# Optimization experiments

Measured on AMD Instinct MI355X. Metric: run time of the kernel, lower is better.

The kernel has to match this reference:

```python
import jax, jax.numpy as jnp
import numpy as np

D_MODEL = 1024
NUM_HEADS = 16
D_K = D_MODEL // NUM_HEADS


def setup_inputs() -> dict:
    key = jax.random.key(0)
    ks = jax.random.split(key, 6)
    B, S = 2, 2048
    scale = 1.0 / np.sqrt(D_MODEL)
    x = jax.random.normal(ks[0], (B, S, D_MODEL), dtype=jnp.float32)
    w_q = jax.random.normal(ks[1], (D_MODEL, D_MODEL), dtype=jnp.float32) * scale
    w_k = jax.random.normal(ks[2], (D_MODEL, D_MODEL), dtype=jnp.float32) * scale
    w_v = jax.random.normal(ks[3], (D_MODEL, D_MODEL), dtype=jnp.float32) * scale
    w_o = jax.random.normal(ks[4], (D_MODEL, D_MODEL), dtype=jnp.float32) * scale
    b_o = jax.random.normal(ks[5], (D_MODEL,), dtype=jnp.float32) * 0.01
    return {"x": x, "w_q": w_q, "w_k": w_k, "w_v": w_v, "w_o": w_o, "b_o": b_o}


def reference(x, w_q, w_k, w_v, w_o, b_o):
    B, S, _ = x.shape
    # Linear(d, d, bias=False): y = x @ W.T ; weights stored torch-style [out, in]
    def proj(w):
        y = jnp.einsum('bsd,ed->bse', x, w)
        return y.reshape(B, S, NUM_HEADS, D_K).transpose(0, 2, 1, 3)  # [B,H,S,Dk]
    Q, K, V = proj(w_q), proj(w_k), proj(w_v)
    scores = jnp.einsum('bhqd,bhkd->bhqk', Q, K) / np.sqrt(D_K)
    attn = jax.nn.softmax(scores, axis=-1)  # dropout p=0 (eval) -> identity
    out = jnp.einsum('bhqk,bhkd->bhqd', attn, V)
    out = out.transpose(0, 2, 1, 3).reshape(B, S, D_MODEL)
    return jnp.einsum('bsd,ed->bse', out, w_o) + b_o
```

## Files before the change

kernel.cpp:

```cpp
#include <hip/hip_runtime.h>
#include <hip/hip_bf16.h>


typedef __bf16 bf16x8 __attribute__((ext_vector_type(8)));
typedef float f32x4 __attribute__((ext_vector_type(4)));

__device__ __forceinline__ unsigned short f2bf(float f) {
  union { float f; unsigned int u; } c; c.f = f;
  unsigned int u = c.u;
  return (unsigned short)((u + 0x7FFFu + ((u >> 16) & 1u)) >> 16);
}

__device__ __forceinline__ unsigned int pk2bf(float a, float b) {
  union { float f; unsigned int u; } x, y;
  x.f = a; y.f = b;
  return __builtin_amdgcn_perm(y.u + 0x8000u, x.u + 0x8000u, 0x07060302u);
}

__device__ __forceinline__ bf16x8 ld_frag(const unsigned short* p) {
  union { uint4 u; bf16x8 b; } c;
  c.u = *(const uint4*)p;
  return c.b;
}

__device__ __forceinline__ uint4 cvt8(const float* __restrict__ p) {
  float4 a = *(const float4*)p;
  float4 b = *(const float4*)(p + 4);
  union { uint4 u; unsigned short s[8]; } r;
  r.s[0] = f2bf(a.x); r.s[1] = f2bf(a.y); r.s[2] = f2bf(a.z); r.s[3] = f2bf(a.w);
  r.s[4] = f2bf(b.x); r.s[5] = f2bf(b.y); r.s[6] = f2bf(b.z); r.s[7] = f2bf(b.w);
  return r.u;
}

typedef __attribute__((address_space(1))) const unsigned int as1_u32;
typedef __attribute__((address_space(3))) unsigned int as3_u32;
__device__ __forceinline__ void async16(const unsigned short* g,
                                        unsigned short* l) {
  __builtin_amdgcn_global_load_lds(
      (as1_u32*)(unsigned long long)g,
      (as3_u32*)(unsigned int)(unsigned long long)l, 16, 0, 0);
}

__global__ __launch_bounds__(256) void cvt_all(
    const float* __restrict__ s0, const float* __restrict__ s1,
    const float* __restrict__ s2, const float* __restrict__ s3,
    const float* __restrict__ s4,
    unsigned short* __restrict__ d0, unsigned short* __restrict__ d1,
    unsigned short* __restrict__ d2, unsigned short* __restrict__ d3,
    unsigned short* __restrict__ d4) {
  const float* srcs[5] = {s0, s1, s2, s3, s4};
  unsigned short* dsts[5] = {d0, d1, d2, d3, d4};
  const int ns[5] = {4194304, 1048576, 1048576, 1048576, 1048576};
  const int y = blockIdx.y;
  const int idx = (blockIdx.x * 256 + threadIdx.x) * 8;
  if (idx >= ns[y]) return;
  *(uint4*)(dsts[y] + idx) = cvt8(srcs[y] + idx);
}

template <int BM, bool OUT_F32>
__global__ __launch_bounds__(256) void gemm_bt(
    const unsigned short* __restrict__ A,
    const unsigned short* __restrict__ w0,
    const unsigned short* __restrict__ w1,
    const unsigned short* __restrict__ w2,
    const float* __restrict__ bias,
    void* __restrict__ outraw, float z0scale) {
  constexpr int NT = (BM == 128) ? 4 : 2;
  const int z = blockIdx.z;
  const unsigned short* W = (z == 0) ? w0 : ((z == 1) ? w1 : w2);
  const float scl = (z == 0) ? z0scale : 1.0f;

  __shared__ unsigned short a_lds[BM * 32];
  __shared__ unsigned short b_lds[128 * 32];

  const int tid = threadIdx.x;
  const int wave = tid >> 6, lane = tid & 63;
  const int quad = lane >> 4, l16 = lane & 15;
  const int wm = (BM == 128) ? (wave >> 1) * 64 : 0;
  const int wn = (BM == 128) ? (wave & 1) * 64 : wave * 32;
  const int bm = blockIdx.y * BM, bn = blockIdx.x * 128;

  const int rl = lane >> 2;
  const int kc = (lane & 3) ^ (rl & 3) ^ ((rl >> 2) & 3);
  const int arow = (BM == 128) ? (wave * 32 + rl) : (wave * 16 + rl);
  const unsigned short* ga = A + (size_t)(bm + arow) * 1024 + kc * 8;
  const unsigned short* gb = W + (size_t)(bn + wave * 32 + rl) * 1024 + kc * 8;
  unsigned short* la = &a_lds[arow - rl + 0] + 0;
  la = &a_lds[((BM == 128) ? wave * 32 : wave * 16) * 32];
  unsigned short* lb = &b_lds[wave * 32 * 32];

  const int rsw8 = ((l16 & 3) ^ ((l16 >> 2) & 3)) * 8;

  f32x4 acc[4][NT] = {};

  for (int k0 = 0; k0 < 1024; k0 += 32) {
    async16(ga, la);
    if (BM == 128) async16(ga + 16 * 1024, la + 16 * 32);
    async16(gb, lb);
    async16(gb + 16 * 1024, lb + 16 * 32);
    ga += 32; gb += 32;
    __syncthreads();

    bf16x8 af[4], bfr[NT];
#pragma unroll
    for (int t = 0; t < 4; ++t)
      af[t] = ld_frag(&a_lds[(wm + t * 16 + l16) * 32 + ((quad * 8) ^ rsw8)]);
#pragma unroll
    for (int t = 0; t < NT; ++t)
      bfr[t] = ld_frag(&b_lds[(wn + t * 16 + l16) * 32 + ((quad * 8) ^ rsw8)]);
#pragma unroll
    for (int mt = 0; mt < 4; ++mt)
#pragma unroll
      for (int nt = 0; nt < NT; ++nt)
        acc[mt][nt] = __builtin_amdgcn_mfma_f32_16x16x32_bf16(
            af[mt], bfr[nt], acc[mt][nt], 0, 0, 0);
    __syncthreads();
  }

#pragma unroll
  for (int nt = 0; nt < NT; ++nt) {
    const int n = bn + wn + nt * 16 + l16;
    const float bv = bias ? bias[n] : 0.0f;
#pragma unroll
    for (int mt = 0; mt < 4; ++mt)
#pragma unroll
      for (int r = 0; r < 4; ++r) {
        const int m = bm + wm + mt * 16 + quad * 4 + r;
        const float v = acc[mt][nt][r] * scl + bv;
        if (OUT_F32)
          ((float*)outraw)[(size_t)z * 4096 * 1024 + (size_t)m * 1024 + n] = v;
        else
          ((unsigned short*)outraw)[(size_t)z * 4096 * 1024 +
                                    (size_t)m * 1024 + n] = f2bf(v);
      }
  }
}

__global__ __launch_bounds__(256) void transpose_v(
    const unsigned short* __restrict__ v, unsigned short* __restrict__ vt) {
  const int st0 = blockIdx.x * 64;
  const int bh = blockIdx.y, b = bh >> 4, h = bh & 15;
  __shared__ unsigned short t[64 * 72];
  const int tid = threadIdx.x;
#pragma unroll
  for (int it = 0; it < 2; ++it) {
    const int c = it * 256 + tid;
    const int row = c >> 3, c8 = (c & 7) * 8;
    *(uint4*)&t[row * 72 + c8] =
        *(const uint4*)(v + (size_t)(b * 2048 + st0 + row) * 1024 + h * 64 + c8);
  }
  __syncthreads();
#pragma unroll
  for (int it = 0; it < 2; ++it) {
    const int c = it * 256 + tid;
    const int drow = c >> 3, s8 = (c & 7) * 8;
    union { uint4 u; unsigned short e[8]; } o;
#pragma unroll
    for (int j = 0; j < 8; ++j) o.e[j] = t[(s8 + j) * 72 + drow];
    *(uint4*)(vt + ((size_t)bh * 64 + drow) * 2048 + st0 + s8) = o.u;
  }
}

__global__ __launch_bounds__(256) void attn3(
    const unsigned short* __restrict__ qkv,
    const unsigned short* __restrict__ vt_g,
    unsigned short* __restrict__ ab) {
  constexpr size_t PL = (size_t)4096 * 1024;
  const int qt = blockIdx.x, bh = blockIdx.y;
  const int b = bh >> 4, h = bh & 15;

  __shared__ unsigned short kp[128 * 136];
  __shared__ unsigned short vtl[64 * 136];

  const int tid = threadIdx.x;
  const int wave = tid >> 6, lane = tid & 63;
  const int quad = lane >> 4, l16 = lane & 15;
  const int qb = quad * 20;

  const unsigned short* Kp = qkv + PL + ((size_t)b * 2048) * 1024 + h * 64;
  const unsigned short* Vt = vt_g + (size_t)bh * 64 * 2048;

  bf16x8 qf[2][2];
#pragma unroll
  for (int hf = 0; hf < 2; ++hf) {
    const unsigned short* qrow =
        qkv + (size_t)(b * 2048 + qt * 128 + wave * 32 + hf * 16 + l16) * 1024 +
        h * 64;
    union { uint4 u; bf16x8 bv; } c;
    c.u = *(const uint4*)(qrow + quad * 8);       qf[hf][0] = c.bv;
    c.u = *(const uint4*)(qrow + 32 + quad * 8);  qf[hf][1] = c.bv;
  }

  f32x4 o_acc[2][4] = {};
  float l_part[2] = {0.0f, 0.0f};

  for (int kv0 = 0; kv0 < 2048; kv0 += 128) {
    __syncthreads();
#pragma unroll
    for (int it = 0; it < 4; ++it) {
      const int c = it * 256 + tid;
      const int kr = c >> 3, kc = (c & 7) * 8;
      *(uint4*)&kp[kr * 72 + kc] =
          *(const uint4*)(Kp + (size_t)(kv0 + kr) * 1024 + kc);
      const int vr = c >> 4, vc = (c & 15) * 8;
      *(uint4*)&vtl[vr * 136 + vc] =
          *(const uint4*)(Vt + (size_t)vr * 2048 + kv0 + vc);
    }
    __syncthreads();

    f32x4 st[2][8] = {};
#pragma unroll
    for (int mb = 0; mb < 8; ++mb) {
      bf16x8 ak0 = ld_frag(&kp[(mb * 16 + l16) * 72 + quad * 8]);
      bf16x8 ak1 = ld_frag(&kp[(mb * 16 + l16) * 72 + 32 + quad * 8]);
#pragma unroll
      for (int hf = 0; hf < 2; ++hf) {
        st[hf][mb] = __builtin_amdgcn_mfma_f32_16x16x32_bf16(
            ak0, qf[hf][0], st[hf][mb], 0, 0, 0);
        st[hf][mb] = __builtin_amdgcn_mfma_f32_16x16x32_bf16(
            ak1, qf[hf][1], st[hf][mb], 0, 0, 0);
      }
    }

#pragma unroll
    for (int hf = 0; hf < 2; ++hf)
#pragma unroll
      for (int mb = 0; mb < 8; ++mb)
#pragma unroll
        for (int r = 0; r < 4; ++r) {
          const float p = __builtin_amdgcn_exp2f(st[hf][mb][r]);
          st[hf][mb][r] = p;
          l_part[hf] += p;
        }

    __syncthreads();
#pragma unroll
    for (int hf = 0; hf < 2; ++hf)
#pragma unroll
      for (int mb = 0; mb < 8; ++mb) {
        uint2 pk;
        pk.x = pk2bf(st[hf][mb][0], st[hf][mb][1]);
        pk.y = pk2bf(st[hf][mb][2], st[hf][mb][3]);
        *(uint2*)&kp[(wave * 32 + hf * 16 + l16) * 136 + mb * 16 + quad * 4] =
            pk;
      }

#pragma unroll
    for (int ks = 0; ks < 4; ++ks) {
      bf16x8 bvf[4];
#pragma unroll
      for (int nt = 0; nt < 4; ++nt)
        bvf[nt] = ld_frag(&vtl[(nt * 16 + l16) * 136 + ks * 32 + quad * 8]);
#pragma unroll
      for (int hf = 0; hf < 2; ++hf) {
        bf16x8 ap =
            ld_frag(&kp[(wave * 32 + hf * 16 + l16) * 136 + ks * 32 + quad * 8]);
#pragma unroll
        for (int nt = 0; nt < 4; ++nt)
          o_acc[hf][nt] = __builtin_amdgcn_mfma_f32_16x16x32_bf16(
              ap, bvf[nt], o_acc[hf][nt], 0, 0, 0);
      }
    }
  }

#pragma unroll
  for (int hf = 0; hf < 2; ++hf) {
    float lp = l_part[hf];
    lp += __shfl_xor(lp, 16);
    lp += __shfl_xor(lp, 32);
    float lr[4];
#pragma unroll
    for (int r = 0; r < 4; ++r) lr[r] = 1.0f / __shfl(lp, qb + r);
#pragma unroll
    for (int nt = 0; nt < 4; ++nt)
#pragma unroll
      for (int r = 0; r < 4; ++r) {
        const int row = qt * 128 + wave * 32 + hf * 16 + quad * 4 + r;
        ab[((size_t)b * 2048 + row) * 1024 + h * 64 + nt * 16 + l16] =
            f2bf(o_acc[hf][nt][r] * lr[r]);
      }
  }
}

extern "C" void kernel_launch(void* const* d_in, const int* in_sizes, int n_in,
                              void* d_out, int out_size, void* d_ws,
                              size_t ws_size, hipStream_t stream) {
  const float* x  = (const float*)d_in[0];
  const float* wq = (const float*)d_in[1];
  const float* wk = (const float*)d_in[2];
  const float* wv = (const float*)d_in[3];
  const float* wo = (const float*)d_in[4];
  const float* bo = (const float*)d_in[5];

  constexpr size_t PL = (size_t)4096 * 1024;
  unsigned short* qkv = (unsigned short*)d_ws;
  unsigned short* ab  = qkv + 2 * PL;
  unsigned short* xb  = qkv + 3 * PL;
  unsigned short* vt  = xb;
  unsigned short* wqb = qkv + 4 * PL;
  unsigned short* wkb = wqb + 1024 * 1024;
  unsigned short* wvb = wkb + 1024 * 1024;
  unsigned short* wob = wvb + 1024 * 1024;

  const float QSCALE = 0.18033688011112042f;

  cvt_all<<<dim3(2048, 5), 256, 0, stream>>>(x, wq, wk, wv, wo,
                                             xb, wqb, wkb, wvb, wob);
  gemm_bt<128, false><<<dim3(8, 32, 3), 256, 0, stream>>>(
      xb, wqb, wkb, wvb, nullptr, qkv, QSCALE);
  transpose_v<<<dim3(32, 32), 256, 0, stream>>>(qkv + 2 * PL, vt);
  attn3<<<dim3(16, 32), 256, 0, stream>>>(qkv, vt, ab);
  gemm_bt<64, true><<<dim3(8, 64, 1), 256, 0, stream>>>(
      ab, wob, wob, wob, bo, d_out, 1.0f);
}
```

Before: 222.4 us.

## Rewrite attention kernel with 32x32 MFMA, split-KV waves and register P

The attention kernel is restructured: each block now handles 64 queries, and its four waves split the KV sequence into two halves, combined at the end through shared memory. It uses 32x32x16 MFMAs, loads K/V tiles with async copies into XOR-swizzled LDS, and keeps the probabilities in registers using permlane32 swaps instead of writing them to LDS. The goal is to remove the P round-trip through LDS and the extra barriers, raise occupancy (launch bounds of 4, a smaller LDS footprint, twice as many blocks) and use wider MFMAs. The cost is a final cross-wave reduction step and more complex indexing.

```diff
diff --git a/kernel.cpp b/kernel.cpp
--- a/kernel.cpp
+++ b/kernel.cpp
@@ -4,6 +4,7 @@
 
 typedef __bf16 bf16x8 __attribute__((ext_vector_type(8)));
 typedef float f32x4 __attribute__((ext_vector_type(4)));
+typedef float f32x16 __attribute__((ext_vector_type(16)));
 
 __device__ __forceinline__ unsigned short f2bf(float f) {
   union { float f; unsigned int u; } c; c.f = f;
@@ -85,8 +86,7 @@
   const int arow = (BM == 128) ? (wave * 32 + rl) : (wave * 16 + rl);
   const unsigned short* ga = A + (size_t)(bm + arow) * 1024 + kc * 8;
   const unsigned short* gb = W + (size_t)(bn + wave * 32 + rl) * 1024 + kc * 8;
-  unsigned short* la = &a_lds[arow - rl + 0] + 0;
-  la = &a_lds[((BM == 128) ? wave * 32 : wave * 16) * 32];
+  unsigned short* la = &a_lds[((BM == 128) ? wave * 32 : wave * 16) * 32];
   unsigned short* lb = &b_lds[wave * 32 * 32];
 
   const int rsw8 = ((l16 & 3) ^ ((l16 >> 2) & 3)) * 8;
@@ -161,7 +161,7 @@
   }
 }
 
-__global__ __launch_bounds__(256) void attn3(
+__global__ __launch_bounds__(256, 4) void attn4(
     const unsigned short* __restrict__ qkv,
     const unsigned short* __restrict__ vt_g,
     unsigned short* __restrict__ ab) {
@@ -169,116 +169,121 @@
   const int qt = blockIdx.x, bh = blockIdx.y;
   const int b = bh >> 4, h = bh & 15;
 
-  __shared__ unsigned short kp[128 * 136];
-  __shared__ unsigned short vtl[64 * 136];
+  __shared__ __align__(16) unsigned short kvs[2][2][64 * 64];
+  __shared__ float sm_l[2][2][32];
 
   const int tid = threadIdx.x;
   const int wave = tid >> 6, lane = tid & 63;
-  const int quad = lane >> 4, l16 = lane & 15;
-  const int qb = quad * 20;
-
-  const unsigned short* Kp = qkv + PL + ((size_t)b * 2048) * 1024 + h * 64;
-  const unsigned short* Vt = vt_g + (size_t)bh * 64 * 2048;
-
-  bf16x8 qf[2][2];
-#pragma unroll
-  for (int hf = 0; hf < 2; ++hf) {
-    const unsigned short* qrow =
-        qkv + (size_t)(b * 2048 + qt * 128 + wave * 32 + hf * 16 + l16) * 1024 +
-        h * 64;
-    union { uint4 u; bf16x8 bv; } c;
-    c.u = *(const uint4*)(qrow + quad * 8);       qf[hf][0] = c.bv;
-    c.u = *(const uint4*)(qrow + 32 + quad * 8);  qf[hf][1] = c.bv;
-  }
-
-  f32x4 o_acc[2][4] = {};
-  float l_part[2] = {0.0f, 0.0f};
-
-  for (int kv0 = 0; kv0 < 2048; kv0 += 128) {
+  const int ws = wave >> 1, wq = wave & 1;
+  const int hi = lane >> 5, l32 = lane & 31;
+  const int row8 = lane >> 3;
+  const int sl = (lane & 7) ^ (row8 & 7);
+  const int swz = (l32 & 7) * 8;
+
+  const unsigned short* qrow =
+      qkv + (size_t)(b * 2048 + qt * 64 + wq * 32 + l32) * 1024 + h * 64 +
+      hi * 8;
+  bf16x8 qf[4];
+#pragma unroll
+  for (int kc = 0; kc < 4; ++kc) qf[kc] = ld_frag(qrow + kc * 16);
+
+  const unsigned short* gK =
+      qkv + PL + (size_t)(b * 2048 + ws * 1024 + wq * 32 + row8) * 1024 +
+      h * 64 + sl * 8;
+  const unsigned short* gV =
+      vt_g + (size_t)bh * 64 * 2048 + (size_t)(wq * 32 + row8) * 2048 +
+      ws * 1024 + sl * 8;
+  unsigned short* lK = &kvs[ws][0][wq * 4 * 512];
+  unsigned short* lV = &kvs[ws][1][wq * 4 * 512];
+
+  f32x16 o_acc[2] = {};
+  float l_part = 0.0f;
+
+  for (int t = 0; t < 16; ++t) {
+#pragma unroll
+    for (int c = 0; c < 4; ++c) {
+      async16(gK + (size_t)c * 8 * 1024, lK + c * 512);
+      async16(gV + (size_t)c * 8 * 2048, lV + c * 512);
+    }
+    gK += 64 * 1024;
+    gV += 64;
     __syncthreads();
-#pragma unroll
-    for (int it = 0; it < 4; ++it) {
-      const int c = it * 256 + tid;
-      const int kr = c >> 3, kc = (c & 7) * 8;
-      *(uint4*)&kp[kr * 72 + kc] =
-          *(const uint4*)(Kp + (size_t)(kv0 + kr) * 1024 + kc);
-      const int vr = c >> 4, vc = (c & 15) * 8;
-      *(uint4*)&vtl[vr * 136 + vc] =
-          *(const uint4*)(Vt + (size_t)vr * 2048 + kv0 + vc);
+
+    f32x16 st[2] = {};
+#pragma unroll
+    for (int mb = 0; mb < 2; ++mb)
+#pragma unroll
+      for (int kc = 0; kc < 4; ++kc) {
+        bf16x8 ak = ld_frag(
+            &kvs[ws][0][(mb * 32 + l32) * 64 + (((2 * kc + hi) * 8) ^ swz)]);
+        st[mb] = __builtin_amdgcn_mfma_f32_32x32x16_bf16(ak, qf[kc], st[mb],
+                                                         0, 0, 0);
+      }
+
+    unsigned int u[2][4][2];
+#pragma unroll
+    for (int mb = 0; mb < 2; ++mb) {
+#pragma unroll
+      for (int r = 0; r < 16; ++r) {
+        const float p = __builtin_amdgcn_exp2f(st[mb][r]);
+        st[mb][r] = p;
+        l_part += p;
+      }
+#pragma unroll
+      for (int g = 0; g < 4; ++g) {
+        u[mb][g][0] = pk2bf(st[mb][g * 4 + 0], st[mb][g * 4 + 1]);
+        u[mb][g][1] = pk2bf(st[mb][g * 4 + 2], st[mb][g * 4 + 3]);
+      }
+    }
+
+#pragma unroll
+    for (int ks = 0; ks < 4; ++ks) {
+      const int m = ks >> 1, g = (ks & 1) * 2;
+      unsigned int a0 = u[m][g][0], b0 = u[m][g + 1][0];
+      unsigned int a1 = u[m][g][1], b1 = u[m][g + 1][1];
+      asm("v_permlane32_swap_b32 %0, %1" : "+v"(a0), "+v"(b0));
+      asm("v_permlane32_swap_b32 %0, %1" : "+v"(a1), "+v"(b1));
+      union { unsigned int w[4]; bf16x8 f; } pa;
+      pa.w[0] = a0; pa.w[1] = a1; pa.w[2] = b0; pa.w[3] = b1;
+#pragma unroll
+      for (int nb = 0; nb < 2; ++nb) {
+        bf16x8 bv = ld_frag(
+            &kvs[ws][1][(nb * 32 + l32) * 64 + (((2 * ks + hi) * 8) ^ swz)]);
+        o_acc[nb] = __builtin_amdgcn_mfma_f32_32x32x16_bf16(pa.f, bv,
+                                                            o_acc[nb], 0, 0, 0);
+      }
     }
     __syncthreads();
-
-    f32x4 st[2][8] = {};
-#pragma unroll
-    for (int mb = 0; mb < 8; ++mb) {
-      bf16x8 ak0 = ld_frag(&kp[(mb * 16 + l16) * 72 + quad * 8]);
-      bf16x8 ak1 = ld_frag(&kp[(mb * 16 + l16) * 72 + 32 + quad * 8]);
-#pragma unroll
-      for (int hf = 0; hf < 2; ++hf) {
-        st[hf][mb] = __builtin_amdgcn_mfma_f32_16x16x32_bf16(
-            ak0, qf[hf][0], st[hf][mb], 0, 0, 0);
-        st[hf][mb] = __builtin_amdgcn_mfma_f32_16x16x32_bf16(
-            ak1, qf[hf][1], st[hf][mb], 0, 0, 0);
+  }
+
+  float lsum = l_part + __shfl_xor(l_part, 32);
+
+  float* sm_o = (float*)&kvs[0][0][0];
+  if (ws == 1) {
+#pragma unroll
+    for (int nb = 0; nb < 2; ++nb)
+#pragma unroll
+      for (int r = 0; r < 16; ++r) {
+        const int q = (r & 3) + 8 * (r >> 2) + 4 * hi;
+        sm_o[wq * 2048 + q * 64 + nb * 32 + l32] = o_acc[nb][r];
+      }
+  }
+  if (lane < 32) sm_l[ws][wq][l32] = lsum;
+  __syncthreads();
+
+  if (ws == 0) {
+#pragma unroll
+    for (int r = 0; r < 16; ++r) {
+      const int q = (r & 3) + 8 * (r >> 2) + 4 * hi;
+      const float inv = 1.0f / (sm_l[0][wq][q] + sm_l[1][wq][q]);
+      const size_t row = (size_t)(b * 2048 + qt * 64 + wq * 32 + q);
+#pragma unroll
+      for (int nb = 0; nb < 2; ++nb) {
+        const float v =
+            (o_acc[nb][r] + sm_o[wq * 2048 + q * 64 + nb * 32 + l32]) * inv;
+        ab[row * 1024 + h * 64 + nb * 32 + l32] = f2bf(v);
       }
     }
-
-#pragma unroll
-    for (int hf = 0; hf < 2; ++hf)
-#pragma unroll
-      for (int mb = 0; mb < 8; ++mb)
-#pragma unroll
-        for (int r = 0; r < 4; ++r) {
-          const float p = __builtin_amdgcn_exp2f(st[hf][mb][r]);
-          st[hf][mb][r] = p;
-          l_part[hf] += p;
-        }
-
-    __syncthreads();
-#pragma unroll
-    for (int hf = 0; hf < 2; ++hf)
-#pragma unroll
-      for (int mb = 0; mb < 8; ++mb) {
-        uint2 pk;
-        pk.x = pk2bf(st[hf][mb][0], st[hf][mb][1]);
-        pk.y = pk2bf(st[hf][mb][2], st[hf][mb][3]);
-        *(uint2*)&kp[(wave * 32 + hf * 16 + l16) * 136 + mb * 16 + quad * 4] =
-            pk;
-      }
-
-#pragma unroll
-    for (int ks = 0; ks < 4; ++ks) {
-      bf16x8 bvf[4];
-#pragma unroll
-      for (int nt = 0; nt < 4; ++nt)
-        bvf[nt] = ld_frag(&vtl[(nt * 16 + l16) * 136 + ks * 32 + quad * 8]);
-#pragma unroll
-      for (int hf = 0; hf < 2; ++hf) {
-        bf16x8 ap =
-            ld_frag(&kp[(wave * 32 + hf * 16 + l16) * 136 + ks * 32 + quad * 8]);
-#pragma unroll
-        for (int nt = 0; nt < 4; ++nt)
-          o_acc[hf][nt] = __builtin_amdgcn_mfma_f32_16x16x32_bf16(
-              ap, bvf[nt], o_acc[hf][nt], 0, 0, 0);
-      }
-    }
-  }
-
-#pragma unroll
-  for (int hf = 0; hf < 2; ++hf) {
-    float lp = l_part[hf];
-    lp += __shfl_xor(lp, 16);
-    lp += __shfl_xor(lp, 32);
-    float lr[4];
-#pragma unroll
-    for (int r = 0; r < 4; ++r) lr[r] = 1.0f / __shfl(lp, qb + r);
-#pragma unroll
-    for (int nt = 0; nt < 4; ++nt)
-#pragma unroll
-      for (int r = 0; r < 4; ++r) {
-        const int row = qt * 128 + wave * 32 + hf * 16 + quad * 4 + r;
-        ab[((size_t)b * 2048 + row) * 1024 + h * 64 + nt * 16 + l16] =
-            f2bf(o_acc[hf][nt][r] * lr[r]);
-      }
   }
 }
 
@@ -309,7 +314,7 @@
   gemm_bt<128, false><<<dim3(8, 32, 3), 256, 0, stream>>>(
       xb, wqb, wkb, wvb, nullptr, qkv, QSCALE);
   transpose_v<<<dim3(32, 32), 256, 0, stream>>>(qkv + 2 * PL, vt);
-  attn3<<<dim3(16, 32), 256, 0, stream>>>(qkv, vt, ab);
+  attn4<<<dim3(32, 32), 256, 0, stream>>>(qkv, vt, ab);
   gemm_bt<64, true><<<dim3(8, 64, 1), 256, 0, stream>>>(
       ab, wob, wob, wob, bo, d_out, 1.0f);
 }
```

Result: faster. 197.4 us (-11.3%).
